# Kernel tuning notes

Measured on AMD Instinct MI355X. Metric: run time of the kernel, lower is better.

## Reference

```python
import jax, jax.numpy as jnp
import numpy as np

B, C, H, W = 4, 64, 128, 128
HEADS = 4
HEAD_DIM = C // HEADS
K = 3          # kernel_size
KK = K * K
PAD = 1        # padding (stride=1 so L == H*W)


def setup_inputs() -> dict:
    key = jax.random.key(0)
    ks = jax.random.split(key, 9)
    s = 0.02
    return {
        "x":  jax.random.normal(ks[0], (B, C, H, W), jnp.float32),
        "fg": jax.random.normal(ks[1], (B, C, H, W), jnp.float32),
        "bg": jax.random.normal(ks[2], (B, C, H, W), jnp.float32),
        # Linear params stored (in, out); y = x @ W + b (equivalent to torch x @ W.T + b)
        "W_v":  jax.random.normal(ks[3], (C, C), jnp.float32) * s,
        "b_v":  jnp.zeros((C,), jnp.float32),
        "W_fg": jax.random.normal(ks[4], (C, KK * KK * HEADS), jnp.float32) * s,
        "b_fg": jnp.zeros((KK * KK * HEADS,), jnp.float32),
        "W_bg": jax.random.normal(ks[5], (C, KK * KK * HEADS), jnp.float32) * s,
        "b_bg": jnp.zeros((KK * KK * HEADS,), jnp.float32),
    }


def _unfold_patches(v_nhwc):
    # v_nhwc: (B,H,W,C) -> (B, H*W, KK, C) matching torch nn.Unfold taps ordering (ki,kj)
    vp = jnp.pad(v_nhwc, ((0, 0), (PAD, PAD), (PAD, PAD), (0, 0)))
    taps = [vp[:, i:i + H, j:j + W, :] for i in range(K) for j in range(K)]
    return jnp.stack(taps, axis=3).reshape(v_nhwc.shape[0], H * W, KK, v_nhwc.shape[-1])


def reference(x, fg, bg, W_v, b_v, W_fg, b_fg, W_bg, b_bg):
    b = x.shape[0]
    x_l = x.transpose(0, 2, 3, 1)              # (B,H,W,C) channel-last
    fg_l = fg.transpose(0, 2, 3, 1).reshape(b, H * W, C)
    bg_l = bg.transpose(0, 2, 3, 1).reshape(b, H * W, C)

    v = x_l @ W_v + b_v                        # (B,H,W,C)
    # unfolded values: (B, L, KK, C) -> (B, heads, L, KK, head_dim)
    patches = _unfold_patches(v).reshape(b, H * W, KK, HEADS, HEAD_DIM)
    patches = patches.transpose(0, 3, 1, 2, 4)

    # per-pixel (KK x KK) attention maps; dropout is identity in eval
    a_fg = (fg_l @ W_fg + b_fg).reshape(b, H * W, HEADS, KK, KK).transpose(0, 2, 1, 3, 4)
    a_bg = (bg_l @ W_bg + b_bg).reshape(b, H * W, HEADS, KK, KK).transpose(0, 2, 1, 3, 4)

    # (attn @ v).sum(dim=3) == sum_j (sum_i attn[..,i,j]) * v[..,j,:]; fg and bg are summed
    attn_total = a_fg.sum(axis=3) + a_bg.sum(axis=3)      # (B, heads, L, KK)
    out = jnp.einsum('bhlj,bhljd->bhld', attn_total, patches)  # (B, heads, L, head_dim)

    # permute to (B, heads, head_dim, L) then reshape to (B,C,H,W) (matches torch reshape)
    return out.transpose(0, 1, 3, 2).reshape(b, C, H, W)
```

## Files before the change

### kernel.cpp

```cpp
#include <hip/hip_runtime.h>
#include <hip/hip_bf16.h>

#define HGT 128
#define WID 128
#define HW  (HGT * WID)
#define CCH 64

#define TILE_W 32
#define TILE_H 4
#define HALO_W 34
#define HALO_H 6
#define NHP    204
#define NGROUP 13
#define VSLOTS 208

typedef __attribute__((ext_vector_type(8))) short bf16x8;
typedef __attribute__((ext_vector_type(4))) float f32x4;
typedef __attribute__((ext_vector_type(4))) unsigned short u16x4;

#define BA_OFF   5120

__device__ inline short f2bf(float f) {
    unsigned u = __float_as_uint(f);
    unsigned r = (u + 0x7fffu + ((u >> 16) & 1u)) >> 16;
    return (short)r;
}
__device__ inline float bf2f(unsigned short u) {
    return __uint_as_float(((unsigned)u) << 16);
}

__global__ void prep_kernel(const float* __restrict__ Wv,
                            const float* __restrict__ Wfg,
                            const float* __restrict__ bfg,
                            const float* __restrict__ Wbg,
                            const float* __restrict__ bbg,
                            float* __restrict__ ws) {
    int idx = blockIdx.x * 256 + threadIdx.x;
    unsigned short* wf = (unsigned short*)ws;
    if (idx < 20 * 64 * 8) {
        int j    = idx & 7;
        int lane = (idx >> 3) & 63;
        int t    = idx >> 9;
        int lo = lane & 15, hi = lane >> 4;
        float val;
        if (t < 8) {
            int nt = t >> 1, kf = t & 1;
            int k = kf * 32 + hi * 8 + j;
            int n = nt * 16 + lo;
            val = Wv[k * 64 + n];
        } else {
            int t2 = t - 8;
            int nt = t2 >> 2, kf = t2 & 3;
            int k = kf * 32 + hi * 8 + j;
            int n = nt * 16 + lo;
            if (n >= 36) {
                val = 0.f;
            } else {
                int h = n / 9, jj = n % 9;
                const float* W = (k < 64) ? Wfg : Wbg;
                int c = (k < 64) ? k : k - 64;
                float s = 0.f;
                #pragma unroll
                for (int i = 0; i < 9; i++) s += W[c * 324 + h * 81 + i * 9 + jj];
                val = s;
            }
        }
        wf[idx] = (unsigned short)f2bf(val);
    } else if (idx < 20 * 64 * 8 + 48) {
        int n = idx - 20 * 64 * 8;
        float s = 0.f;
        if (n < 36) {
            int h = n / 9, jj = n % 9;
            #pragma unroll
            for (int i = 0; i < 9; i++)
                s += bfg[h * 81 + i * 9 + jj] + bbg[h * 81 + i * 9 + jj];
        }
        ws[BA_OFF + n] = s;
    }
}

__global__ __launch_bounds__(256, 2) void fused_kernel(
        const float* __restrict__ x, const float* __restrict__ fg,
        const float* __restrict__ bg, const float* __restrict__ bv,
        const float* __restrict__ ws, float* __restrict__ out) {
    __shared__ unsigned short v_lds[VSLOTS * 64];
    __shared__ float attn_lds[TILE_W * TILE_H * 37];

    int tid  = threadIdx.x;
    int wave = tid >> 6, lane = tid & 63;
    int lo = lane & 15, hi = lane >> 4;

    int bid = blockIdx.x;
    int b  = bid >> 7;
    int t  = bid & 127;
    int ty = t >> 2, tx = t & 3;
    int y0 = ty * TILE_H, x0 = tx * TILE_W;
    const size_t bin = (size_t)b * CCH * HW;
    const unsigned short* wf = (const unsigned short*)ws;

    bf16x8 a1[8];
    #pragma unroll
    for (int tt = 0; tt < 8; tt++)
        a1[tt] = *(const bf16x8*)(wf + ((size_t)tt * 64 + lane) * 8);

    float xr0[16], xr1[16], xr2[16], xr3[16];
    int hp_[4];

#define ISSUE_X(gi, dst)                                                      \
    {                                                                         \
        int g = (gi) * 4 + wave;                                              \
        if (g < NGROUP) {                                                     \
            int hp = g * 16 + lo;                                             \
            hp_[gi] = hp;                                                     \
            int hps = min(hp, NHP - 1);                                       \
            int rr = hps / HALO_W;                                            \
            int cc = hps - rr * HALO_W;                                       \
            int yy = min(max(y0 - 1 + rr, 0), HGT - 1);                       \
            int xx = min(max(x0 - 1 + cc, 0), WID - 1);                       \
            const float* xp = x + bin + yy * WID + xx;                        \
            _Pragma("unroll")                                                 \
            for (int q = 0; q < 16; q++)                                      \
                dst[q] = xp[(size_t)((q >> 3) * 32 + hi * 8 + (q & 7)) * HW]; \
        }                                                                     \
    }

    ISSUE_X(0, xr0)
    ISSUE_X(1, xr1)
    ISSUE_X(2, xr2)
    ISSUE_X(3, xr3)

    float fr0[16], gr0[16];
    {
        int ip = wave * 16 + lo;
        int r = ip >> 5, c = ip & 31;
        const float* fp = fg + bin + (size_t)(y0 + r) * WID + x0 + c;
        const float* gp = bg + bin + (size_t)(y0 + r) * WID + x0 + c;
        #pragma unroll
        for (int q = 0; q < 16; q++)
            fr0[q] = fp[(size_t)((q >> 3) * 32 + hi * 8 + (q & 7)) * HW];
        #pragma unroll
        for (int q = 0; q < 16; q++)
            gr0[q] = gp[(size_t)((q >> 3) * 32 + hi * 8 + (q & 7)) * HW];
    }

#define P1_COMPUTE(gi, src)                                                   \
    {                                                                         \
        int g = (gi) * 4 + wave;                                              \
        if (g < NGROUP) {                                                     \
            bf16x8 bx0, bx1;                                                  \
            _Pragma("unroll")                                                 \
            for (int j = 0; j < 8; j++) {                                     \
                bx0[j] = f2bf(src[j]);                                        \
                bx1[j] = f2bf(src[8 + j]);                                    \
            }                                                                 \
            f32x4 av[4];                                                      \
            _Pragma("unroll")                                                 \
            for (int nt = 0; nt < 4; nt++)                                    \
                _Pragma("unroll")                                             \
                for (int r = 0; r < 4; r++)                                   \
                    av[nt][r] = bv[nt * 16 + hi * 4 + r];                     \
            _Pragma("unroll")                                                 \
            for (int nt = 0; nt < 4; nt++) {                                  \
                av[nt] = __builtin_amdgcn_mfma_f32_16x16x32_bf16(a1[nt * 2 + 0], bx0, av[nt], 0, 0, 0); \
                av[nt] = __builtin_amdgcn_mfma_f32_16x16x32_bf16(a1[nt * 2 + 1], bx1, av[nt], 0, 0, 0); \
            }                                                                 \
            char* vb = (char*)v_lds;                                          \
            int hp = hp_[gi];                                                 \
            _Pragma("unroll")                                                 \
            for (int nt = 0; nt < 4; nt++) {                                  \
                u16x4 pk;                                                     \
                _Pragma("unroll")                                             \
                for (int r = 0; r < 4; r++) pk[r] = (unsigned short)f2bf(av[nt][r]); \
                int byte = hp * 128 + ((nt * 32 + hi * 8) ^ ((hp & 7) << 4)); \
                *(u16x4*)(vb + byte) = pk;                                    \
            }                                                                 \
        }                                                                     \
    }

    P1_COMPUTE(0, xr0)
    P1_COMPUTE(1, xr1)
    P1_COMPUTE(2, xr2)
    P1_COMPUTE(3, xr3)

    float fr1[16], gr1[16];
    {
        int ip = 64 + wave * 16 + lo;
        int r = ip >> 5, c = ip & 31;
        const float* fp = fg + bin + (size_t)(y0 + r) * WID + x0 + c;
        const float* gp = bg + bin + (size_t)(y0 + r) * WID + x0 + c;
        #pragma unroll
        for (int q = 0; q < 16; q++)
            fr1[q] = fp[(size_t)((q >> 3) * 32 + hi * 8 + (q & 7)) * HW];
        #pragma unroll
        for (int q = 0; q < 16; q++)
            gr1[q] = gp[(size_t)((q >> 3) * 32 + hi * 8 + (q & 7)) * HW];
    }
    bf16x8 a2[12];
    #pragma unroll
    for (int tt = 0; tt < 12; tt++)
        a2[tt] = *(const bf16x8*)(wf + ((size_t)(8 + tt) * 64 + lane) * 8);

#define P2_COMPUTE(ipexpr, fr, gr)                                            \
    {                                                                         \
        int ip = (ipexpr);                                                    \
        bf16x8 b2_[4];                                                        \
        _Pragma("unroll")                                                     \
        for (int j = 0; j < 8; j++) {                                         \
            b2_[0][j] = f2bf(fr[j]);                                          \
            b2_[1][j] = f2bf(fr[8 + j]);                                      \
            b2_[2][j] = f2bf(gr[j]);                                          \
            b2_[3][j] = f2bf(gr[8 + j]);                                      \
        }                                                                     \
        f32x4 aa[3];                                                          \
        _Pragma("unroll")                                                     \
        for (int nt = 0; nt < 3; nt++)                                        \
            _Pragma("unroll")                                                 \
            for (int r4 = 0; r4 < 4; r4++)                                    \
                aa[nt][r4] = ws[BA_OFF + nt * 16 + hi * 4 + r4];              \
        _Pragma("unroll")                                                     \
        for (int nt = 0; nt < 3; nt++)                                        \
            _Pragma("unroll")                                                 \
            for (int kf = 0; kf < 4; kf++)                                    \
                aa[nt] = __builtin_amdgcn_mfma_f32_16x16x32_bf16(a2[nt * 4 + kf], b2_[kf], aa[nt], 0, 0, 0); \
        float* ab = attn_lds + ip * 37;                                       \
        *(f32x4*)(ab + hi * 4)      = aa[0];                                  \
        *(f32x4*)(ab + 16 + hi * 4) = aa[1];                                  \
        if (hi == 0) *(f32x4*)(ab + 32) = aa[2];                              \
    }

    P2_COMPUTE(wave * 16 + lo, fr0, gr0)
    P2_COMPUTE(64 + wave * 16 + lo, fr1, gr1)

    __syncthreads();

    {
        int ip    = tid & 127;
        int hpair = tid >> 7;
        int r = ip >> 5, c = ip & 31;
        int y = y0 + r, xq = x0 + c;

        float acc[32];
        #pragma unroll
        for (int o = 0; o < 32; o++) acc[o] = 0.f;

        const char* vb = (const char*)v_lds;
        const float* ab = attn_lds + ip * 37 + hpair * 18;

        #pragma unroll
        for (int j = 0; j < 9; j++) {
            int dy = j / 3 - 1, dx = j % 3 - 1;
            bool valid = (unsigned)(y + dy) < HGT && (unsigned)(xq + dx) < WID;
            int tp = (r + 1 + dy) * HALO_W + (c + 1 + dx);
            float w0 = valid ? ab[j] : 0.f;
            float w1 = valid ? ab[9 + j] : 0.f;

            int base = tp * 128;
            int sw = (tp & 7) << 4;
            int k0 = hpair * 4;
            bf16x8 ch0 = *(const bf16x8*)(vb + base + (((k0 + 0) * 16) ^ sw));
            bf16x8 ch1 = *(const bf16x8*)(vb + base + (((k0 + 1) * 16) ^ sw));
            bf16x8 ch2 = *(const bf16x8*)(vb + base + (((k0 + 2) * 16) ^ sw));
            bf16x8 ch3 = *(const bf16x8*)(vb + base + (((k0 + 3) * 16) ^ sw));
            #pragma unroll
            for (int e = 0; e < 8; e++) {
                acc[e]      += w0 * bf2f((unsigned short)ch0[e]);
                acc[8 + e]  += w0 * bf2f((unsigned short)ch1[e]);
                acc[16 + e] += w1 * bf2f((unsigned short)ch2[e]);
                acc[24 + e] += w1 * bf2f((unsigned short)ch3[e]);
            }
        }

        float* ob = out + bin + (size_t)(hpair * 32) * HW + (size_t)y * WID + xq;
        #pragma unroll
        for (int o = 0; o < 32; o++)
            ob[(size_t)o * HW] = acc[o];
    }
}

extern "C" void kernel_launch(void* const* d_in, const int* in_sizes, int n_in,
                              void* d_out, int out_size, void* d_ws, size_t ws_size,
                              hipStream_t stream) {
    const float* x   = (const float*)d_in[0];
    const float* fg  = (const float*)d_in[1];
    const float* bg  = (const float*)d_in[2];
    const float* Wv  = (const float*)d_in[3];
    const float* bv  = (const float*)d_in[4];
    const float* Wfg = (const float*)d_in[5];
    const float* bfg = (const float*)d_in[6];
    const float* Wbg = (const float*)d_in[7];
    const float* bbg = (const float*)d_in[8];

    float* ws  = (float*)d_ws;
    float* out = (float*)d_out;

    prep_kernel<<<41, 256, 0, stream>>>(Wv, Wfg, bfg, Wbg, bbg, ws);

    fused_kernel<<<512, 256, 0, stream>>>(x, fg, bg, bv, ws, out);
}
```

Before: 30.32 us.

## Cut register pressure for three blocks per CU and remap block order

Raises the launch-bounds occupancy target from 2 to 3 blocks per CU. To fit, the x loads are restructured into a two-buffer load/compute ping-pong instead of prefetching all four groups at once, and fg/bg loads move into each attention-compute step, which shrinks live registers. Block indices are also permuted so consecutive blocks fall on different tiles and batches. The trade is less memory-level parallelism within each wave, in exchange for more resident waves to hide latency, plus a risk of spills under the tighter register cap.

Result: faster. 25.85 us (-14.7%).

```diff
diff --git a/kernel.cpp b/kernel.cpp
--- a/kernel.cpp
+++ b/kernel.cpp
@@ -79,7 +79,7 @@
     }
 }
 
-__global__ __launch_bounds__(256, 2) void fused_kernel(
+__global__ __launch_bounds__(256, 3) void fused_kernel(
         const float* __restrict__ x, const float* __restrict__ fg,
         const float* __restrict__ bg, const float* __restrict__ bv,
         const float* __restrict__ ws, float* __restrict__ out) {
@@ -90,7 +90,9 @@
     int wave = tid >> 6, lane = tid & 63;
     int lo = lane & 15, hi = lane >> 4;
 
-    int bid = blockIdx.x;
+    int bid0 = blockIdx.x;
+    int bid  = (bid0 & 7) * 64 + (bid0 >> 3);
+
     int b  = bid >> 7;
     int t  = bid & 127;
     int ty = t >> 2, tx = t & 3;
@@ -98,55 +100,29 @@
     const size_t bin = (size_t)b * CCH * HW;
     const unsigned short* wf = (const unsigned short*)ws;
 
-    bf16x8 a1[8];
-    #pragma unroll
-    for (int tt = 0; tt < 8; tt++)
-        a1[tt] = *(const bf16x8*)(wf + ((size_t)tt * 64 + lane) * 8);
-
-    float xr0[16], xr1[16], xr2[16], xr3[16];
-    int hp_[4];
-
-#define ISSUE_X(gi, dst)                                                      \
+#define LOAD_G(dst, g)                                                        \
     {                                                                         \
-        int g = (gi) * 4 + wave;                                              \
-        if (g < NGROUP) {                                                     \
-            int hp = g * 16 + lo;                                             \
-            hp_[gi] = hp;                                                     \
-            int hps = min(hp, NHP - 1);                                       \
-            int rr = hps / HALO_W;                                            \
-            int cc = hps - rr * HALO_W;                                       \
-            int yy = min(max(y0 - 1 + rr, 0), HGT - 1);                       \
-            int xx = min(max(x0 - 1 + cc, 0), WID - 1);                       \
-            const float* xp = x + bin + yy * WID + xx;                        \
-            _Pragma("unroll")                                                 \
-            for (int q = 0; q < 16; q++)                                      \
-                dst[q] = xp[(size_t)((q >> 3) * 32 + hi * 8 + (q & 7)) * HW]; \
-        }                                                                     \
-    }
-
-    ISSUE_X(0, xr0)
-    ISSUE_X(1, xr1)
-    ISSUE_X(2, xr2)
-    ISSUE_X(3, xr3)
-
-    float fr0[16], gr0[16];
+        int hp = (g) * 16 + lo;                                               \
+        int hps = min(hp, NHP - 1);                                           \
+        int rr = hps / HALO_W;                                                \
+        int cc = hps - rr * HALO_W;                                           \
+        int yy = min(max(y0 - 1 + rr, 0), HGT - 1);                           \
+        int xx = min(max(x0 - 1 + cc, 0), WID - 1);                           \
+        const float* xp = x + bin + yy * WID + xx;                            \
+        _Pragma("unroll")                                                     \
+        for (int q = 0; q < 16; q++)                                          \
+            dst[q] = xp[(size_t)((q >> 3) * 32 + hi * 8 + (q & 7)) * HW];     \
+    }
+
     {
-        int ip = wave * 16 + lo;
-        int r = ip >> 5, c = ip & 31;
-        const float* fp = fg + bin + (size_t)(y0 + r) * WID + x0 + c;
-        const float* gp = bg + bin + (size_t)(y0 + r) * WID + x0 + c;
-        #pragma unroll
-        for (int q = 0; q < 16; q++)
-            fr0[q] = fp[(size_t)((q >> 3) * 32 + hi * 8 + (q & 7)) * HW];
-        #pragma unroll
-        for (int q = 0; q < 16; q++)
-            gr0[q] = gp[(size_t)((q >> 3) * 32 + hi * 8 + (q & 7)) * HW];
-    }
-
-#define P1_COMPUTE(gi, src)                                                   \
-    {                                                                         \
-        int g = (gi) * 4 + wave;                                              \
-        if (g < NGROUP) {                                                     \
+        bf16x8 a1[8];
+        #pragma unroll
+        for (int tt = 0; tt < 8; tt++)
+            a1[tt] = *(const bf16x8*)(wf + ((size_t)tt * 64 + lane) * 8);
+
+#define COMP_G(src, g)                                                        \
+        {                                                                     \
+            int hp = (g) * 16 + lo;                                           \
             bf16x8 bx0, bx1;                                                  \
             _Pragma("unroll")                                                 \
             for (int j = 0; j < 8; j++) {                                     \
@@ -165,7 +141,6 @@
                 av[nt] = __builtin_amdgcn_mfma_f32_16x16x32_bf16(a1[nt * 2 + 1], bx1, av[nt], 0, 0, 0); \
             }                                                                 \
             char* vb = (char*)v_lds;                                          \
-            int hp = hp_[gi];                                                 \
             _Pragma("unroll")                                                 \
             for (int nt = 0; nt < 4; nt++) {                                  \
                 u16x4 pk;                                                     \
@@ -174,62 +149,66 @@
                 int byte = hp * 128 + ((nt * 32 + hi * 8) ^ ((hp & 7) << 4)); \
                 *(u16x4*)(vb + byte) = pk;                                    \
             }                                                                 \
-        }                                                                     \
-    }
-
-    P1_COMPUTE(0, xr0)
-    P1_COMPUTE(1, xr1)
-    P1_COMPUTE(2, xr2)
-    P1_COMPUTE(3, xr3)
-
-    float fr1[16], gr1[16];
+        }
+
+        float xrA[16], xrB[16];
+        LOAD_G(xrA, wave)
+        LOAD_G(xrB, 4 + wave)
+        COMP_G(xrA, wave)
+        LOAD_G(xrA, 8 + wave)
+        COMP_G(xrB, 4 + wave)
+        if (wave == 0) LOAD_G(xrB, 12)
+        COMP_G(xrA, 8 + wave)
+        if (wave == 0) COMP_G(xrB, 12)
+    }
+
     {
-        int ip = 64 + wave * 16 + lo;
-        int r = ip >> 5, c = ip & 31;
-        const float* fp = fg + bin + (size_t)(y0 + r) * WID + x0 + c;
-        const float* gp = bg + bin + (size_t)(y0 + r) * WID + x0 + c;
-        #pragma unroll
-        for (int q = 0; q < 16; q++)
-            fr1[q] = fp[(size_t)((q >> 3) * 32 + hi * 8 + (q & 7)) * HW];
-        #pragma unroll
-        for (int q = 0; q < 16; q++)
-            gr1[q] = gp[(size_t)((q >> 3) * 32 + hi * 8 + (q & 7)) * HW];
-    }
-    bf16x8 a2[12];
-    #pragma unroll
-    for (int tt = 0; tt < 12; tt++)
-        a2[tt] = *(const bf16x8*)(wf + ((size_t)(8 + tt) * 64 + lane) * 8);
-
-#define P2_COMPUTE(ipexpr, fr, gr)                                            \
-    {                                                                         \
-        int ip = (ipexpr);                                                    \
-        bf16x8 b2_[4];                                                        \
-        _Pragma("unroll")                                                     \
-        for (int j = 0; j < 8; j++) {                                         \
-            b2_[0][j] = f2bf(fr[j]);                                          \
-            b2_[1][j] = f2bf(fr[8 + j]);                                      \
-            b2_[2][j] = f2bf(gr[j]);                                          \
-            b2_[3][j] = f2bf(gr[8 + j]);                                      \
-        }                                                                     \
-        f32x4 aa[3];                                                          \
-        _Pragma("unroll")                                                     \
-        for (int nt = 0; nt < 3; nt++)                                        \
-            _Pragma("unroll")                                                 \
-            for (int r4 = 0; r4 < 4; r4++)                                    \
-                aa[nt][r4] = ws[BA_OFF + nt * 16 + hi * 4 + r4];              \
-        _Pragma("unroll")                                                     \
-        for (int nt = 0; nt < 3; nt++)                                        \
-            _Pragma("unroll")                                                 \
-            for (int kf = 0; kf < 4; kf++)                                    \
-                aa[nt] = __builtin_amdgcn_mfma_f32_16x16x32_bf16(a2[nt * 4 + kf], b2_[kf], aa[nt], 0, 0, 0); \
-        float* ab = attn_lds + ip * 37;                                       \
-        *(f32x4*)(ab + hi * 4)      = aa[0];                                  \
-        *(f32x4*)(ab + 16 + hi * 4) = aa[1];                                  \
-        if (hi == 0) *(f32x4*)(ab + 32) = aa[2];                              \
-    }
-
-    P2_COMPUTE(wave * 16 + lo, fr0, gr0)
-    P2_COMPUTE(64 + wave * 16 + lo, fr1, gr1)
+        bf16x8 a2[12];
+        #pragma unroll
+        for (int tt = 0; tt < 12; tt++)
+            a2[tt] = *(const bf16x8*)(wf + ((size_t)(8 + tt) * 64 + lane) * 8);
+
+#define P2_COMPUTE(ipexpr)                                                    \
+        {                                                                     \
+            int ip = (ipexpr);                                                \
+            int r = ip >> 5, c = ip & 31;                                     \
+            const float* fp = fg + bin + (size_t)(y0 + r) * WID + x0 + c;     \
+            const float* gp = bg + bin + (size_t)(y0 + r) * WID + x0 + c;     \
+            float fr[16], gr[16];                                             \
+            _Pragma("unroll")                                                 \
+            for (int q = 0; q < 16; q++)                                      \
+                fr[q] = fp[(size_t)((q >> 3) * 32 + hi * 8 + (q & 7)) * HW];  \
+            _Pragma("unroll")                                                 \
+            for (int q = 0; q < 16; q++)                                      \
+                gr[q] = gp[(size_t)((q >> 3) * 32 + hi * 8 + (q & 7)) * HW];  \
+            bf16x8 b2_[4];                                                    \
+            _Pragma("unroll")                                                 \
+            for (int j = 0; j < 8; j++) {                                     \
+                b2_[0][j] = f2bf(fr[j]);                                      \
+                b2_[1][j] = f2bf(fr[8 + j]);                                  \
+                b2_[2][j] = f2bf(gr[j]);                                      \
+                b2_[3][j] = f2bf(gr[8 + j]);                                  \
+            }                                                                 \
+            f32x4 aa[3];                                                      \
+            _Pragma("unroll")                                                 \
+            for (int nt = 0; nt < 3; nt++)                                    \
+                _Pragma("unroll")                                             \
+                for (int r4 = 0; r4 < 4; r4++)                                \
+                    aa[nt][r4] = ws[BA_OFF + nt * 16 + hi * 4 + r4];          \
+            _Pragma("unroll")                                                 \
+            for (int nt = 0; nt < 3; nt++)                                    \
+                _Pragma("unroll")                                             \
+                for (int kf = 0; kf < 4; kf++)                                \
+                    aa[nt] = __builtin_amdgcn_mfma_f32_16x16x32_bf16(a2[nt * 4 + kf], b2_[kf], aa[nt], 0, 0, 0); \
+            float* ab = attn_lds + ip * 37;                                   \
+            *(f32x4*)(ab + hi * 4)      = aa[0];                              \
+            *(f32x4*)(ab + 16 + hi * 4) = aa[1];                              \
+            if (hi == 0) *(f32x4*)(ab + 32) = aa[2];                          \
+        }
+
+        P2_COMPUTE(wave * 16 + lo)
+        P2_COMPUTE(64 + wave * 16 + lo)
+    }
 
     __syncthreads();
 
```
